# Kernel tuning notes

Hardware: AMD Instinct MI355X
Metric: run time of the kernel (lower is better)

Reference implementation:

```python
import math
import jax, jax.numpy as jnp
import numpy as np

FACTOR = 3  # AutoCorrelation(factor=3)

def reference(queries, keys, values):
    # queries/keys/values: [B, L, D]; source requires L == S for the broadcast below.
    B, L, D = queries.shape
    S = keys.shape[1]
    # NOTE (faithful to source): rfft is over the LAST axis with fft_length L/S,
    # i.e. the feature axis D is zero-padded (or truncated) to length L.
    q_fft = jnp.fft.rfft(queries, n=L, axis=-1)          # [B, L, L//2+1] complex
    k_fft = jnp.fft.rfft(keys, n=S, axis=-1)             # [B, S, S//2+1] complex
    corr = jnp.fft.irfft(q_fft * jnp.conj(k_fft), n=L + S - 1, axis=-1)  # [B, L, L+S-1]

    top_k = int(FACTOR * math.log(float(L)))
    mean_value = jnp.mean(corr, axis=1)                  # [B, L+S-1]
    top_k = min(top_k, mean_value.shape[-1])
    top_k_val, top_k_ind = jax.lax.top_k(mean_value, top_k)  # [B, K]
    tmp_corr = jax.nn.softmax(top_k_val, axis=-1)        # [B, K]

    # Faithful to source: the roll shift for every batch element uses the
    # delays of batch element 0 (index[0] in the TF loop).
    shifts = top_k_ind[0]                                # [K] int32
    # Vectorized replacement of the per-index tf.roll loop.
    V_rolled = jax.vmap(lambda s: jnp.roll(values, -s, axis=1))(shifts)  # [K, B, L, D]
    # Weighted aggregation over the K retained delays (intended semantics of
    # the source einsum, which as written has a rank mismatch).
    output = jnp.einsum('kbld,bk->bld', V_rolled, tmp_corr)  # [B, L, D]
    return output

def setup_inputs() -> dict:
    key = jax.random.key(0)
    k1, k2, k3 = jax.random.split(key, 3)
    B, L, D = 8, 1024, 512
    return {
        'queries': jax.random.normal(k1, (B, L, D), dtype=jnp.float32),
        'keys':    jax.random.normal(k2, (B, L, D), dtype=jnp.float32),
        'values':  jax.random.normal(k3, (B, L, D), dtype=jnp.float32),
    }
```

## Files before the change

### kernel.cpp

```cpp
#include <hip/hip_runtime.h>
#include <math.h>

#define NB 8
#define NL 1024
#define ND 512
#define NF 513
#define NT 2047
#define TOPK 20

typedef __attribute__((ext_vector_type(8))) short short8;
typedef __attribute__((ext_vector_type(4))) float f32x4;

static __device__ __forceinline__ unsigned short bf16_rne(float x) {
    unsigned int u = __builtin_bit_cast(unsigned int, x);
    unsigned int r = (u + 0x7fffu + ((u >> 16) & 1u)) >> 16;
    return (unsigned short)r;
}
static __device__ __forceinline__ float bf16_to_f(unsigned short h) {
    unsigned int u = ((unsigned int)h) << 16;
    return __builtin_bit_cast(float, u);
}

__global__ __launch_bounds__(256) void k_tr(const float* __restrict__ q,
                                            const float* __restrict__ kk,
                                            unsigned short* __restrict__ Thi,
                                            unsigned short* __restrict__ Tlo) {
    __shared__ float tile[64][65];
    const int which = blockIdx.z;
    const int b  = blockIdx.y;
    const int l0 = (blockIdx.x & 15) * 64;
    const int d0 = (blockIdx.x >> 4) * 64;
    const float* src = (which ? kk : q) + (size_t)b * NL * ND;
    const int t = threadIdx.x;
    const int r = t >> 4, c = t & 15;
    #pragma unroll
    for (int rr = 0; rr < 4; ++rr) {
        const float4 v = *(const float4*)&src[(size_t)(l0 + r + 16 * rr) * ND + d0 + c * 4];
        tile[r + 16 * rr][c * 4 + 0] = v.x;
        tile[r + 16 * rr][c * 4 + 1] = v.y;
        tile[r + 16 * rr][c * 4 + 2] = v.z;
        tile[r + 16 * rr][c * 4 + 3] = v.w;
    }
    __syncthreads();
    unsigned short* hi = Thi + ((size_t)which * NB + b) * (size_t)ND * NL;
    unsigned short* lo = Tlo + ((size_t)which * NB + b) * (size_t)ND * NL;
    #pragma unroll
    for (int p = 0; p < 2; ++p) {
        const int c2 = t + 256 * p;
        const int dl = c2 >> 3;
        const int l8 = (c2 & 7) * 8;
        short8 vh, vl;
        #pragma unroll
        for (int i = 0; i < 8; ++i) {
            const float x = tile[l8 + i][dl];
            const unsigned short h = bf16_rne(x);
            vh[i] = (short)h;
            vl[i] = (short)bf16_rne(x - bf16_to_f(h));
        }
        *(short8*)&hi[(size_t)(d0 + dl) * NL + l0 + l8] = vh;
        *(short8*)&lo[(size_t)(d0 + dl) * NL + l0 + l8] = vl;
    }
}

#define GBK 64
#define GPAD 8
#define GKT 4

__global__ __launch_bounds__(256, 2) void k_gemm(const unsigned short* __restrict__ Thi,
                                                 const unsigned short* __restrict__ Tlo,
                                                 float* __restrict__ S) {
    __shared__ unsigned short Ahi[128][GBK + GPAD];
    __shared__ unsigned short Alo[128][GBK + GPAD];
    __shared__ unsigned short Bhi[128][GBK + GPAD];
    __shared__ unsigned short Blo[128][GBK + GPAD];
    __shared__ float sd4[4][256];
    const int id   = blockIdx.x;
    const int b    = id & 7;
    const int rest = id >> 3;
    const int mt = rest & 3, nt = (rest >> 2) & 3, kq = rest >> 4;
    const int tid  = threadIdx.x;
    const int lane = tid & 63, w = tid >> 6;
    const int wr = w >> 1, wc = w & 1;
    const int m = lane & 15, g = lane >> 4;

    const size_t plane = (size_t)ND * NL;
    const unsigned short* qhi = Thi + (size_t)b * plane;
    const unsigned short* khi = Thi + ((size_t)NB + b) * plane;
    const unsigned short* qlo = Tlo + (size_t)b * plane;
    const unsigned short* klo = Tlo + ((size_t)NB + b) * plane;

    f32x4 acc[4][4];
    #pragma unroll
    for (int i = 0; i < 4; ++i)
        #pragma unroll
        for (int j = 0; j < 4; ++j) acc[i][j] = (f32x4)(0.f);

    const int kbase = kq * GKT;
    short8 r_ah[4], r_al[4], r_bh[4], r_bl[4];
    #pragma unroll
    for (int p = 0; p < 4; ++p) {
        const int cc  = tid + 256 * p;
        const int row = cc >> 3, col8 = (cc & 7) * 8;
        const size_t ga = (size_t)(mt * 128 + row) * NL + kbase * GBK + col8;
        const size_t gb = (size_t)(nt * 128 + row) * NL + kbase * GBK + col8;
        r_ah[p] = *(const short8*)&qhi[ga];
        r_al[p] = *(const short8*)&qlo[ga];
        r_bh[p] = *(const short8*)&khi[gb];
        r_bl[p] = *(const short8*)&klo[gb];
    }

    for (int kt = 0; kt < GKT; ++kt) {
        __syncthreads();
        #pragma unroll
        for (int p = 0; p < 4; ++p) {
            const int cc  = tid + 256 * p;
            const int row = cc >> 3, col8 = (cc & 7) * 8;
            *(short8*)&Ahi[row][col8] = r_ah[p];
            *(short8*)&Alo[row][col8] = r_al[p];
            *(short8*)&Bhi[row][col8] = r_bh[p];
            *(short8*)&Blo[row][col8] = r_bl[p];
        }
        __syncthreads();
        if (kt + 1 < GKT) {
            #pragma unroll
            for (int p = 0; p < 4; ++p) {
                const int cc  = tid + 256 * p;
                const int row = cc >> 3, col8 = (cc & 7) * 8;
                const size_t ga = (size_t)(mt * 128 + row) * NL + (kbase + kt + 1) * GBK + col8;
                const size_t gb = (size_t)(nt * 128 + row) * NL + (kbase + kt + 1) * GBK + col8;
                r_ah[p] = *(const short8*)&qhi[ga];
                r_al[p] = *(const short8*)&qlo[ga];
                r_bh[p] = *(const short8*)&khi[gb];
                r_bl[p] = *(const short8*)&klo[gb];
            }
        }
        #pragma unroll
        for (int ks = 0; ks < 2; ++ks) {
            short8 ah[4], al[4], bh[4], bl[4];
            #pragma unroll
            for (int i = 0; i < 4; ++i) {
                ah[i] = *(const short8*)&Ahi[wr * 64 + i * 16 + m][ks * 32 + g * 8];
                al[i] = *(const short8*)&Alo[wr * 64 + i * 16 + m][ks * 32 + g * 8];
            }
            #pragma unroll
            for (int j = 0; j < 4; ++j) {
                bh[j] = *(const short8*)&Bhi[wc * 64 + j * 16 + m][ks * 32 + g * 8];
                bl[j] = *(const short8*)&Blo[wc * 64 + j * 16 + m][ks * 32 + g * 8];
            }
            #pragma unroll
            for (int i = 0; i < 4; ++i)
                #pragma unroll
                for (int j = 0; j < 4; ++j) {
                    acc[i][j] = __builtin_amdgcn_mfma_f32_16x16x32_bf16(ah[i], bh[j], acc[i][j], 0, 0, 0);
                    acc[i][j] = __builtin_amdgcn_mfma_f32_16x16x32_bf16(ah[i], bl[j], acc[i][j], 0, 0, 0);
                    acc[i][j] = __builtin_amdgcn_mfma_f32_16x16x32_bf16(al[i], bh[j], acc[i][j], 0, 0, 0);
                }
        }
    }

    for (int i = tid; i < 1024; i += 256) ((float*)sd4)[i] = 0.f;
    __syncthreads();
    float bin[7][4];
    #pragma unroll
    for (int u = 0; u < 7; ++u)
        #pragma unroll
        for (int r2 = 0; r2 < 4; ++r2) bin[u][r2] = 0.f;
    #pragma unroll
    for (int i = 0; i < 4; ++i)
        #pragma unroll
        for (int j = 0; j < 4; ++j)
            #pragma unroll
            for (int r2 = 0; r2 < 4; ++r2) bin[i - j + 3][r2] += acc[i][j][r2];
    const int basei = (wr - wc) * 64 + g * 4 - m + 127;
    #pragma unroll
    for (int u = 0; u < 7; ++u)
        #pragma unroll
        for (int r2 = 0; r2 < 4; ++r2)
            atomicAdd(&sd4[w][basei + (u - 3) * 16 + r2], bin[u][r2]);
    __syncthreads();
    const int doff = (mt - nt) * 128 + 511 - 127;
    if (tid < 255) {
        const float vsum = sd4[0][tid] + sd4[1][tid] + sd4[2][tid] + sd4[3][tid];
        atomicAdd(&S[b * 1023 + doff + tid], vsum);
    }
}

__global__ __launch_bounds__(64) void k_pdft(const float* __restrict__ S,
                                             float* __restrict__ pbar) {
    const int b = blockIdx.y;
    const int f = blockIdx.x;
    const int lane = threadIdx.x;
    const float w = 2.0f * 3.14159265358979323846f / 1024.0f;
    float re = 0.f, im = 0.f;
    #pragma unroll
    for (int i = 0; i < 16; ++i) {
        const int j = lane + 64 * i;
        if (j < 1023) {
            const int mm = (f * (j - 511)) & 1023;
            float s, c;
            sincosf(w * (float)mm, &s, &c);
            const float x = S[b * 1023 + j];
            re = fmaf(x, c, re);
            im = fmaf(x, -s, im);
        }
    }
    #pragma unroll
    for (int off = 32; off; off >>= 1) {
        re += __shfl_xor(re, off);
        im += __shfl_xor(im, off);
    }
    if (lane == 0) {
        pbar[b * 2 * NF + 2 * f]     = re;
        pbar[b * 2 * NF + 2 * f + 1] = im;
    }
}

__global__ __launch_bounds__(256) void k_mean(const float* __restrict__ pbar,
                                              float* __restrict__ mv) {
    __shared__ float P[2 * NF];
    const int b = blockIdx.y;
    for (int i = threadIdx.x; i < 2 * NF; i += 256)
        P[i] = pbar[(size_t)b * (2 * NF) + i];
    __syncthreads();
    const int wave = threadIdx.x >> 6, lane = threadIdx.x & 63;
    const int t = blockIdx.x * 4 + wave;
    if (t >= NT) return;
    const float w2 = 2.0f * 3.14159265358979323846f / 2047.0f;
    float acc = 0.f;
    #pragma unroll
    for (int i = 0; i < 8; ++i) {
        const int f = 1 + lane + 64 * i;
        const int mm = (f * t) % 2047;
        float s, c;
        sincosf(w2 * (float)mm, &s, &c);
        acc = fmaf(P[2 * f], c, acc);
        acc = fmaf(-P[2 * f + 1], s, acc);
    }
    acc *= 2.0f;
    #pragma unroll
    for (int off = 32; off; off >>= 1) acc += __shfl_xor(acc, off);
    if (lane == 0)
        mv[(size_t)b * NT + t] = (acc + P[0]) * (1.0f / (2047.0f * 1024.0f));
}

__global__ __launch_bounds__(256) void k_topk(const float* __restrict__ mv,
                                              float* __restrict__ wts,
                                              int* __restrict__ shifts) {
    __shared__ float v[NT];
    __shared__ float topv[TOPK];
    __shared__ int   topi[TOPK];
    __shared__ float wv[4];
    __shared__ int   wi[4];
    const int b = blockIdx.x;
    const int t = threadIdx.x;
    const int lane = t & 63, wave = t >> 6;
    for (int i = t; i < NT; i += 256) v[i] = mv[(size_t)b * NT + i];
    __syncthreads();
    for (int kkk = 0; kkk < TOPK; ++kkk) {
        float bv = -INFINITY; int bi = 0x7fffffff;
        #pragma unroll
        for (int s = 0; s < 8; ++s) {
            const int i = t + 256 * s;
            if (i < NT) {
                const float x = v[i];
                if (x > bv) { bv = x; bi = i; }
            }
        }
        #pragma unroll
        for (int off = 32; off; off >>= 1) {
            const float ov = __shfl_down(bv, off);
            const int   oi = __shfl_down(bi, off);
            if (ov > bv || (ov == bv && oi < bi)) { bv = ov; bi = oi; }
        }
        if (lane == 0) { wv[wave] = bv; wi[wave] = bi; }
        __syncthreads();
        if (t == 0) {
            bv = wv[0]; bi = wi[0];
            #pragma unroll
            for (int ww = 1; ww < 4; ++ww)
                if (wv[ww] > bv || (wv[ww] == bv && wi[ww] < bi)) { bv = wv[ww]; bi = wi[ww]; }
            topv[kkk] = bv; topi[kkk] = bi;
            v[bi] = -INFINITY;
        }
        __syncthreads();
    }
    if (t == 0) {
        float m = topv[0], sum = 0.f, e[TOPK];
        #pragma unroll
        for (int i = 0; i < TOPK; ++i) { e[i] = expf(topv[i] - m); sum += e[i]; }
        #pragma unroll
        for (int i = 0; i < TOPK; ++i) wts[b * TOPK + i] = e[i] / sum;
        if (b == 0) {
            #pragma unroll
            for (int i = 0; i < TOPK; ++i) shifts[i] = topi[i];
        }
    }
}

__global__ __launch_bounds__(128) void k_out(const float* __restrict__ vals,
                                             const float* __restrict__ wts,
                                             const int* __restrict__ shifts,
                                             float* __restrict__ out) {
    __shared__ float w[TOPK];
    __shared__ int   sh[TOPK];
    const int id = blockIdx.x;
    const int b = id & 7;
    const int l = id >> 3;
    const int t = threadIdx.x;
    if (t < TOPK) { w[t] = wts[b * TOPK + t]; sh[t] = shifts[t]; }
    __syncthreads();
    float4 acc = make_float4(0.f, 0.f, 0.f, 0.f);
    const float4* vb = (const float4*)(vals + (size_t)b * NL * ND);
    #pragma unroll 4
    for (int kkk = 0; kkk < TOPK; ++kkk) {
        const int sl = (l + sh[kkk]) & (NL - 1);
        const float4 x = vb[(size_t)sl * (ND / 4) + t];
        const float wk = w[kkk];
        acc.x = fmaf(wk, x.x, acc.x);
        acc.y = fmaf(wk, x.y, acc.y);
        acc.z = fmaf(wk, x.z, acc.z);
        acc.w = fmaf(wk, x.w, acc.w);
    }
    ((float4*)out)[((size_t)b * NL + l) * (ND / 4) + t] = acc;
}

extern "C" void kernel_launch(void* const* d_in, const int* in_sizes, int n_in,
                              void* d_out, int out_size, void* d_ws, size_t ws_size,
                              hipStream_t stream) {
    const float* q = (const float*)d_in[0];
    const float* k = (const float*)d_in[1];
    const float* v = (const float*)d_in[2];
    float* out    = (float*)d_out;

    const size_t plane = (size_t)ND * NL;
    unsigned short* Thi = (unsigned short*)d_ws;
    unsigned short* Tlo = Thi + 2 * NB * plane;
    float* S      = (float*)(Tlo + 2 * NB * plane);
    float* pbar   = S + NB * 1023;
    float* mv     = pbar + NB * 2 * NF;
    float* wts    = mv + NB * NT;
    int*   shifts = (int*)(wts + NB * TOPK);

    hipMemsetAsync(S, 0, NB * 1023 * sizeof(float), stream);
    k_tr  <<<dim3(128, NB, 2), 256, 0, stream>>>(q, k, Thi, Tlo);
    k_gemm<<<512, 256, 0, stream>>>(Thi, Tlo, S);
    k_pdft<<<dim3(NF, NB), 64, 0, stream>>>(S, pbar);
    k_mean<<<dim3(512, NB), 256, 0, stream>>>(pbar, mv);
    k_topk<<<NB, 256, 0, stream>>>(mv, wts, shifts);
    k_out <<<NL * NB, 128, 0, stream>>>(v, wts, shifts, out);
}
```

Baseline: 185.2 us.

## Fold DFT pair into closed-form Dirichlet kernel and split GEMM K finer

Replaces the two-stage forward DFT plus inverse DFT (k_pdft then k_mean) with a single kernel that applies a closed-form Dirichlet-kernel weight directly to the diagonal sums S, removing one launch and the intermediate spectrum buffer. Zeroing of S moves from hipMemsetAsync into k_tr. The GEMM K tile shrinks from 64 to 32 with 1024 blocks and occupancy hint 3, which gives more parallelism but twice as many atomic flushes into S. The closed form relies on integer modular arithmetic and sinpif ratios, which risks precision differences near singular points.

New measurement: 231.5 us. 25.0% more time.

```diff
diff --git a/kernel.cpp b/kernel.cpp
--- a/kernel.cpp
+++ b/kernel.cpp
@@ -4,9 +4,9 @@
 #define NB 8
 #define NL 1024
 #define ND 512
-#define NF 513
 #define NT 2047
 #define TOPK 20
+#define LMOD 2096128
 
 typedef __attribute__((ext_vector_type(8))) short short8;
 typedef __attribute__((ext_vector_type(4))) float f32x4;
@@ -24,14 +24,18 @@
 __global__ __launch_bounds__(256) void k_tr(const float* __restrict__ q,
                                             const float* __restrict__ kk,
                                             unsigned short* __restrict__ Thi,
-                                            unsigned short* __restrict__ Tlo) {
+                                            unsigned short* __restrict__ Tlo,
+                                            float* __restrict__ S) {
     __shared__ float tile[64][65];
     const int which = blockIdx.z;
     const int b  = blockIdx.y;
     const int l0 = (blockIdx.x & 15) * 64;
     const int d0 = (blockIdx.x >> 4) * 64;
+    const int t = threadIdx.x;
+    if (which == 0 && blockIdx.x == 0) {
+        for (int i = t; i < 1023; i += 256) S[b * 1023 + i] = 0.f;
+    }
     const float* src = (which ? kk : q) + (size_t)b * NL * ND;
-    const int t = threadIdx.x;
     const int r = t >> 4, c = t & 15;
     #pragma unroll
     for (int rr = 0; rr < 4; ++rr) {
@@ -62,11 +66,11 @@
     }
 }
 
-#define GBK 64
+#define GBK 32
 #define GPAD 8
 #define GKT 4
 
-__global__ __launch_bounds__(256, 2) void k_gemm(const unsigned short* __restrict__ Thi,
+__global__ __launch_bounds__(256, 3) void k_gemm(const unsigned short* __restrict__ Thi,
                                                  const unsigned short* __restrict__ Tlo,
                                                  float* __restrict__ S) {
     __shared__ unsigned short Ahi[128][GBK + GPAD];
@@ -96,11 +100,11 @@
         for (int j = 0; j < 4; ++j) acc[i][j] = (f32x4)(0.f);
 
     const int kbase = kq * GKT;
-    short8 r_ah[4], r_al[4], r_bh[4], r_bl[4];
-    #pragma unroll
-    for (int p = 0; p < 4; ++p) {
+    short8 r_ah[2], r_al[2], r_bh[2], r_bl[2];
+    #pragma unroll
+    for (int p = 0; p < 2; ++p) {
         const int cc  = tid + 256 * p;
-        const int row = cc >> 3, col8 = (cc & 7) * 8;
+        const int row = cc >> 2, col8 = (cc & 3) * 8;
         const size_t ga = (size_t)(mt * 128 + row) * NL + kbase * GBK + col8;
         const size_t gb = (size_t)(nt * 128 + row) * NL + kbase * GBK + col8;
         r_ah[p] = *(const short8*)&qhi[ga];
@@ -112,9 +116,9 @@
     for (int kt = 0; kt < GKT; ++kt) {
         __syncthreads();
         #pragma unroll
-        for (int p = 0; p < 4; ++p) {
+        for (int p = 0; p < 2; ++p) {
             const int cc  = tid + 256 * p;
-            const int row = cc >> 3, col8 = (cc & 7) * 8;
+            const int row = cc >> 2, col8 = (cc & 3) * 8;
             *(short8*)&Ahi[row][col8] = r_ah[p];
             *(short8*)&Alo[row][col8] = r_al[p];
             *(short8*)&Bhi[row][col8] = r_bh[p];
@@ -123,9 +127,9 @@
         __syncthreads();
         if (kt + 1 < GKT) {
             #pragma unroll
-            for (int p = 0; p < 4; ++p) {
+            for (int p = 0; p < 2; ++p) {
                 const int cc  = tid + 256 * p;
-                const int row = cc >> 3, col8 = (cc & 7) * 8;
+                const int row = cc >> 2, col8 = (cc & 3) * 8;
                 const size_t ga = (size_t)(mt * 128 + row) * NL + (kbase + kt + 1) * GBK + col8;
                 const size_t gb = (size_t)(nt * 128 + row) * NL + (kbase + kt + 1) * GBK + col8;
                 r_ah[p] = *(const short8*)&qhi[ga];
@@ -134,28 +138,25 @@
                 r_bl[p] = *(const short8*)&klo[gb];
             }
         }
-        #pragma unroll
-        for (int ks = 0; ks < 2; ++ks) {
-            short8 ah[4], al[4], bh[4], bl[4];
-            #pragma unroll
-            for (int i = 0; i < 4; ++i) {
-                ah[i] = *(const short8*)&Ahi[wr * 64 + i * 16 + m][ks * 32 + g * 8];
-                al[i] = *(const short8*)&Alo[wr * 64 + i * 16 + m][ks * 32 + g * 8];
+        short8 ah[4], al[4], bh[4], bl[4];
+        #pragma unroll
+        for (int i = 0; i < 4; ++i) {
+            ah[i] = *(const short8*)&Ahi[wr * 64 + i * 16 + m][g * 8];
+            al[i] = *(const short8*)&Alo[wr * 64 + i * 16 + m][g * 8];
+        }
+        #pragma unroll
+        for (int j = 0; j < 4; ++j) {
+            bh[j] = *(const short8*)&Bhi[wc * 64 + j * 16 + m][g * 8];
+            bl[j] = *(const short8*)&Blo[wc * 64 + j * 16 + m][g * 8];
+        }
+        #pragma unroll
+        for (int i = 0; i < 4; ++i)
+            #pragma unroll
+            for (int j = 0; j < 4; ++j) {
+                acc[i][j] = __builtin_amdgcn_mfma_f32_16x16x32_bf16(ah[i], bh[j], acc[i][j], 0, 0, 0);
+                acc[i][j] = __builtin_amdgcn_mfma_f32_16x16x32_bf16(ah[i], bl[j], acc[i][j], 0, 0, 0);
+                acc[i][j] = __builtin_amdgcn_mfma_f32_16x16x32_bf16(al[i], bh[j], acc[i][j], 0, 0, 0);
             }
-            #pragma unroll
-            for (int j = 0; j < 4; ++j) {
-                bh[j] = *(const short8*)&Bhi[wc * 64 + j * 16 + m][ks * 32 + g * 8];
-                bl[j] = *(const short8*)&Blo[wc * 64 + j * 16 + m][ks * 32 + g * 8];
-            }
-            #pragma unroll
-            for (int i = 0; i < 4; ++i)
-                #pragma unroll
-                for (int j = 0; j < 4; ++j) {
-                    acc[i][j] = __builtin_amdgcn_mfma_f32_16x16x32_bf16(ah[i], bh[j], acc[i][j], 0, 0, 0);
-                    acc[i][j] = __builtin_amdgcn_mfma_f32_16x16x32_bf16(ah[i], bl[j], acc[i][j], 0, 0, 0);
-                    acc[i][j] = __builtin_amdgcn_mfma_f32_16x16x32_bf16(al[i], bh[j], acc[i][j], 0, 0, 0);
-                }
-        }
     }
 
     for (int i = tid; i < 1024; i += 256) ((float*)sd4)[i] = 0.f;
@@ -185,62 +186,41 @@
     }
 }
 
-__global__ __launch_bounds__(64) void k_pdft(const float* __restrict__ S,
-                                             float* __restrict__ pbar) {
+__global__ __launch_bounds__(256) void k_mean2(const float* __restrict__ S,
+                                               float* __restrict__ mv) {
+    __shared__ float sh[1023];
     const int b = blockIdx.y;
-    const int f = blockIdx.x;
-    const int lane = threadIdx.x;
-    const float w = 2.0f * 3.14159265358979323846f / 1024.0f;
-    float re = 0.f, im = 0.f;
+    for (int i = threadIdx.x; i < 1023; i += 256) sh[i] = S[b * 1023 + i];
+    __syncthreads();
+    const int wave = threadIdx.x >> 6, lane = threadIdx.x & 63;
+    const int t = blockIdx.x * 4 + wave;
+    if (t >= NT) return;
+    const float invL = 1.0f / (float)LMOD;
+    float acc = 0.f;
     #pragma unroll
     for (int i = 0; i < 16; ++i) {
         const int j = lane + 64 * i;
         if (j < 1023) {
-            const int mm = (f * (j - 511)) & 1023;
-            float s, c;
-            sincosf(w * (float)mm, &s, &c);
-            const float x = S[b * 1023 + j];
-            re = fmaf(x, c, re);
-            im = fmaf(x, -s, im);
-        }
-    }
-    #pragma unroll
-    for (int off = 32; off; off >>= 1) {
-        re += __shfl_xor(re, off);
-        im += __shfl_xor(im, off);
-    }
-    if (lane == 0) {
-        pbar[b * 2 * NF + 2 * f]     = re;
-        pbar[b * 2 * NF + 2 * f + 1] = im;
-    }
-}
-
-__global__ __launch_bounds__(256) void k_mean(const float* __restrict__ pbar,
-                                              float* __restrict__ mv) {
-    __shared__ float P[2 * NF];
-    const int b = blockIdx.y;
-    for (int i = threadIdx.x; i < 2 * NF; i += 256)
-        P[i] = pbar[(size_t)b * (2 * NF) + i];
-    __syncthreads();
-    const int wave = threadIdx.x >> 6, lane = threadIdx.x & 63;
-    const int t = blockIdx.x * 4 + wave;
-    if (t >= NT) return;
-    const float w2 = 2.0f * 3.14159265358979323846f / 2047.0f;
-    float acc = 0.f;
-    #pragma unroll
-    for (int i = 0; i < 8; ++i) {
-        const int f = 1 + lane + 64 * i;
-        const int mm = (f * t) % 2047;
-        float s, c;
-        sincosf(w2 * (float)mm, &s, &c);
-        acc = fmaf(P[2 * f], c, acc);
-        acc = fmaf(-P[2 * f + 1], s, acc);
-    }
-    acc *= 2.0f;
+            int un = t * 1024 + (511 - j) * 2047;
+            un %= LMOD; if (un < 0) un += LMOD;
+            float D;
+            if (un == 0) {
+                D = 1025.f;
+            } else {
+                const int un2 = (un > LMOD / 2) ? un - LMOD : un;
+                long long yy = ((long long)un * 1025LL) % (2LL * LMOD);
+                if (yy >= LMOD) yy -= 2LL * LMOD;
+                const float num = sinpif((float)yy * invL);
+                const float den = fabsf(sinpif((float)un2 * invL));
+                D = num / den;
+            }
+            acc = fmaf(sh[j], D, acc);
+        }
+    }
     #pragma unroll
     for (int off = 32; off; off >>= 1) acc += __shfl_xor(acc, off);
     if (lane == 0)
-        mv[(size_t)b * NT + t] = (acc + P[0]) * (1.0f / (2047.0f * 1024.0f));
+        mv[(size_t)b * NT + t] = acc * (1.0f / (2047.0f * 1024.0f));
 }
 
 __global__ __launch_bounds__(256) void k_topk(const float* __restrict__ mv,
@@ -336,16 +316,13 @@
     unsigned short* Thi = (unsigned short*)d_ws;
     unsigned short* Tlo = Thi + 2 * NB * plane;
     float* S      = (float*)(Tlo + 2 * NB * plane);
-    float* pbar   = S + NB * 1023;
-    float* mv     = pbar + NB * 2 * NF;
+    float* mv     = S + NB * 1023;
     float* wts    = mv + NB * NT;
     int*   shifts = (int*)(wts + NB * TOPK);
 
-    hipMemsetAsync(S, 0, NB * 1023 * sizeof(float), stream);
-    k_tr  <<<dim3(128, NB, 2), 256, 0, stream>>>(q, k, Thi, Tlo);
-    k_gemm<<<512, 256, 0, stream>>>(Thi, Tlo, S);
-    k_pdft<<<dim3(NF, NB), 64, 0, stream>>>(S, pbar);
-    k_mean<<<dim3(512, NB), 256, 0, stream>>>(pbar, mv);
-    k_topk<<<NB, 256, 0, stream>>>(mv, wts, shifts);
-    k_out <<<NL * NB, 128, 0, stream>>>(v, wts, shifts, out);
-}
+    k_tr   <<<dim3(128, NB, 2), 256, 0, stream>>>(q, k, Thi, Tlo, S);
+    k_gemm <<<1024, 256, 0, stream>>>(Thi, Tlo, S);
+    k_mean2<<<dim3(512, NB), 256, 0, stream>>>(S, mv);
+    k_topk <<<NB, 256, 0, stream>>>(mv, wts, shifts);
+    k_out  <<<NL * NB, 128, 0, stream>>>(v, wts, shifts, out);
+}
```
